# Optimization experiments

Hardware: AMD Instinct MI355X
Metric: run time of the kernel (lower is better)

The kernel has to match this reference:

```python
import jax, jax.numpy as jnp
import numpy as np

BATCH, IN_F, OUT_F = 128, 2048, 512

def setup_inputs() -> dict:
    key = jax.random.key(0)
    k1, k2 = jax.random.split(key)
    m = jax.random.uniform(k1, (BATCH, IN_F), dtype=jnp.float32)
    # weight drawn slightly outside [0,1] so the clamp preprocessing is exercised
    weight = jax.random.uniform(k2, (IN_F, OUT_F), dtype=jnp.float32) * 1.5 - 0.25
    return {"m": m, "weight": weight}

def reference(m, weight):
    # wf = clamp: constrain weights to [0, 1]
    w = jnp.clip(weight, 0.0, 1.0)
    # f = max_min (tropical 'or' composition):
    # out[b, o] = max_i min(m[b, i], w[i, o])
    # broadcast [B, I, 1] with [1, I, O] then reduce over I
    return jnp.max(jnp.minimum(m[:, :, None], w[None, :, :]), axis=1)
```

## Files before the change

### kernel.cpp

```cpp
#include <hip/hip_runtime.h>


__global__ __launch_bounds__(256)
void tmm(const float* __restrict__ M, const float* __restrict__ W,
         float* __restrict__ out) {
    const int t  = threadIdx.x;
    const int wv = __builtin_amdgcn_readfirstlane(t >> 6);
    const int l  = t & 63;
    const int bid = blockIdx.x;
    const int bb = bid & 7;
    const int ob = (bid >> 3) & 7;
    const int ig = bid >> 6;
    const int b0 = bb * 16 + wv * 4;
    const int oc = ob * 64 + l;
    const int i0 = ig * 128;

    const float* Wp = W + i0 * 512 + oc;
    const float* Mp = M + b0 * 2048 + i0;

    float a0 = 0.f, a1 = 0.f, a2 = 0.f, a3 = 0.f;

#pragma unroll 16
    for (int i = 0; i < 128; ++i) {
        float w  = Wp[i * 512];
        float m0 = Mp[i];
        float m1 = Mp[2048 + i];
        float m2 = Mp[4096 + i];
        float m3 = Mp[6144 + i];
        a0 = fmaxf(a0, fminf(m0, w));
        a1 = fmaxf(a1, fminf(m1, w));
        a2 = fmaxf(a2, fminf(m2, w));
        a3 = fmaxf(a3, fminf(m3, w));
    }

    int* o = (int*)out + b0 * 512 + oc;
    atomicMax(o,            __float_as_int(a0));
    atomicMax(o + 512,      __float_as_int(a1));
    atomicMax(o + 1024,     __float_as_int(a2));
    atomicMax(o + 1536,     __float_as_int(a3));
}

extern "C" void kernel_launch(void* const* d_in, const int* in_sizes, int n_in,
                              void* d_out, int out_size, void* d_ws, size_t ws_size,
                              hipStream_t stream) {
    const float* M = (const float*)d_in[0];
    const float* W = (const float*)d_in[1];
    float* out = (float*)d_out;
    tmm<<<dim3(1024), dim3(256), 0, stream>>>(M, W, out);
}
```

Before: 19.49 us.

## Use 2x4 register tile with float4 loads and finer reduction split

Each thread now computes a 2-row by 4-column output tile over a 64-wide slice of the reduction, using float4 loads for both M and W. This raises the number of max/min updates per load and widens memory accesses, aiming to cut load-instruction overhead. The block shape moves to 512 threads across 512 blocks. Halving the reduction slice doubles the number of atomicMax operations on the output, which adds atomic traffic in exchange.

```diff
diff --git a/kernel.cpp b/kernel.cpp
--- a/kernel.cpp
+++ b/kernel.cpp
@@ -1,43 +1,54 @@
 #include <hip/hip_runtime.h>
 
 
-__global__ __launch_bounds__(256)
+#define UPD(acc, mv, wv)                          \
+    acc.x = fmaxf(acc.x, fminf(mv, wv.x));        \
+    acc.y = fmaxf(acc.y, fminf(mv, wv.y));        \
+    acc.z = fmaxf(acc.z, fminf(mv, wv.z));        \
+    acc.w = fmaxf(acc.w, fminf(mv, wv.w));
+
+__global__ __launch_bounds__(512, 4)
 void tmm(const float* __restrict__ M, const float* __restrict__ W,
          float* __restrict__ out) {
     const int t  = threadIdx.x;
-    const int wv = __builtin_amdgcn_readfirstlane(t >> 6);
-    const int l  = t & 63;
+    const int wv = t >> 6, l = t & 63;
     const int bid = blockIdx.x;
     const int bb = bid & 7;
-    const int ob = (bid >> 3) & 7;
-    const int ig = bid >> 6;
-    const int b0 = bb * 16 + wv * 4;
-    const int oc = ob * 64 + l;
-    const int i0 = ig * 128;
+    const int ob = (bid >> 3) & 1;
+    const int ig = bid >> 4;
+    const int r0 = bb * 16 + wv * 2;
+    const int c0 = ob * 256 + l * 4;
+    const int i0 = ig * 64;
 
-    const float* Wp = W + i0 * 512 + oc;
-    const float* Mp = M + b0 * 2048 + i0;
+    const float* Wp = W + (size_t)i0 * 512 + c0;
+    const float* M0 = M + (size_t)r0 * 2048 + i0;
+    const float* M1 = M0 + 2048;
 
-    float a0 = 0.f, a1 = 0.f, a2 = 0.f, a3 = 0.f;
+    float4 a0 = make_float4(0.f, 0.f, 0.f, 0.f);
+    float4 a1 = make_float4(0.f, 0.f, 0.f, 0.f);
 
-#pragma unroll 16
-    for (int i = 0; i < 128; ++i) {
-        float w  = Wp[i * 512];
-        float m0 = Mp[i];
-        float m1 = Mp[2048 + i];
-        float m2 = Mp[4096 + i];
-        float m3 = Mp[6144 + i];
-        a0 = fmaxf(a0, fminf(m0, w));
-        a1 = fmaxf(a1, fminf(m1, w));
-        a2 = fmaxf(a2, fminf(m2, w));
-        a3 = fmaxf(a3, fminf(m3, w));
+#pragma unroll 4
+    for (int i4 = 0; i4 < 16; ++i4) {
+        float4 m0 = *(const float4*)&M0[i4 * 4];
+        float4 m1 = *(const float4*)&M1[i4 * 4];
+        float4 w0 = *(const float4*)&Wp[(i4 * 4 + 0) * 512];
+        float4 w1 = *(const float4*)&Wp[(i4 * 4 + 1) * 512];
+        float4 w2 = *(const float4*)&Wp[(i4 * 4 + 2) * 512];
+        float4 w3 = *(const float4*)&Wp[(i4 * 4 + 3) * 512];
+        UPD(a0, m0.x, w0)  UPD(a0, m0.y, w1)  UPD(a0, m0.z, w2)  UPD(a0, m0.w, w3)
+        UPD(a1, m1.x, w0)  UPD(a1, m1.y, w1)  UPD(a1, m1.z, w2)  UPD(a1, m1.w, w3)
     }
 
-    int* o = (int*)out + b0 * 512 + oc;
-    atomicMax(o,            __float_as_int(a0));
-    atomicMax(o + 512,      __float_as_int(a1));
-    atomicMax(o + 1024,     __float_as_int(a2));
-    atomicMax(o + 1536,     __float_as_int(a3));
+    int* o0 = (int*)out + r0 * 512 + c0;
+    int* o1 = o0 + 512;
+    atomicMax(o0,     __float_as_int(a0.x));
+    atomicMax(o0 + 1, __float_as_int(a0.y));
+    atomicMax(o0 + 2, __float_as_int(a0.z));
+    atomicMax(o0 + 3, __float_as_int(a0.w));
+    atomicMax(o1,     __float_as_int(a1.x));
+    atomicMax(o1 + 1, __float_as_int(a1.y));
+    atomicMax(o1 + 2, __float_as_int(a1.z));
+    atomicMax(o1 + 3, __float_as_int(a1.w));
 }
 
 extern "C" void kernel_launch(void* const* d_in, const int* in_sizes, int n_in,
@@ -46,5 +57,5 @@
     const float* M = (const float*)d_in[0];
     const float* W = (const float*)d_in[1];
     float* out = (float*)d_out;
-    tmm<<<dim3(1024), dim3(256), 0, stream>>>(M, W, out);
+    tmm<<<dim3(512), dim3(512), 0, stream>>>(M, W, out);
 }
```

New measurement: 50.24 us. 2.58x slower.

## Replace split-K atomics with in-block LDS reduction over full K

Applied to the files above, without the earlier changes.

The grid changes from 1024 blocks of 256 threads to 256 blocks of 512 threads. Each block now covers 4 batch rows by 64 outputs over the whole input dimension, with its 8 waves splitting K and combining partial maxima through shared memory. Each output gets one plain store, so the global atomicMax calls and the reliance on a zero-initialised output buffer are gone, and M is read with float4 loads. The cost is less reuse of W: each loaded weight now serves only 4 batch rows instead of 16, which multiplies weight traffic, and there are fewer waves per CU to hide latency.

```diff
diff --git a/kernel.cpp b/kernel.cpp
--- a/kernel.cpp
+++ b/kernel.cpp
@@ -1,43 +1,55 @@
 #include <hip/hip_runtime.h>
 
 
-__global__ __launch_bounds__(256)
+__global__ __launch_bounds__(512)
 void tmm(const float* __restrict__ M, const float* __restrict__ W,
          float* __restrict__ out) {
-    const int t  = threadIdx.x;
-    const int wv = __builtin_amdgcn_readfirstlane(t >> 6);
-    const int l  = t & 63;
+    __shared__ float part[8][4][64];
+    const int t = threadIdx.x;
+    const int c = t & 63;
+    const int s = t >> 6;
     const int bid = blockIdx.x;
-    const int bb = bid & 7;
-    const int ob = (bid >> 3) & 7;
-    const int ig = bid >> 6;
-    const int b0 = bb * 16 + wv * 4;
-    const int oc = ob * 64 + l;
-    const int i0 = ig * 128;
+    const int ot = bid & 7, bt = bid >> 3;
+    const int b0 = bt * 4, o0 = ot * 64;
 
-    const float* Wp = W + i0 * 512 + oc;
-    const float* Mp = M + b0 * 2048 + i0;
+    const float* Wp = W + (size_t)(s * 256) * 512 + o0 + c;
+    const float* Mp = M + (size_t)b0 * 2048 + s * 256;
 
     float a0 = 0.f, a1 = 0.f, a2 = 0.f, a3 = 0.f;
 
-#pragma unroll 16
-    for (int i = 0; i < 128; ++i) {
-        float w  = Wp[i * 512];
-        float m0 = Mp[i];
-        float m1 = Mp[2048 + i];
-        float m2 = Mp[4096 + i];
-        float m3 = Mp[6144 + i];
-        a0 = fmaxf(a0, fminf(m0, w));
-        a1 = fmaxf(a1, fminf(m1, w));
-        a2 = fmaxf(a2, fminf(m2, w));
-        a3 = fmaxf(a3, fminf(m3, w));
+#pragma unroll 2
+    for (int st = 0; st < 64; ++st) {
+        float4 m0 = *(const float4*)&Mp[st * 4];
+        float4 m1 = *(const float4*)&Mp[2048 + st * 4];
+        float4 m2 = *(const float4*)&Mp[4096 + st * 4];
+        float4 m3 = *(const float4*)&Mp[6144 + st * 4];
+        float w0 = Wp[(st * 4 + 0) * 512];
+        float w1 = Wp[(st * 4 + 1) * 512];
+        float w2 = Wp[(st * 4 + 2) * 512];
+        float w3 = Wp[(st * 4 + 3) * 512];
+        a0 = fmaxf(a0, fminf(m0.x, w0)); a1 = fmaxf(a1, fminf(m1.x, w0));
+        a2 = fmaxf(a2, fminf(m2.x, w0)); a3 = fmaxf(a3, fminf(m3.x, w0));
+        a0 = fmaxf(a0, fminf(m0.y, w1)); a1 = fmaxf(a1, fminf(m1.y, w1));
+        a2 = fmaxf(a2, fminf(m2.y, w1)); a3 = fmaxf(a3, fminf(m3.y, w1));
+        a0 = fmaxf(a0, fminf(m0.z, w2)); a1 = fmaxf(a1, fminf(m1.z, w2));
+        a2 = fmaxf(a2, fminf(m2.z, w2)); a3 = fmaxf(a3, fminf(m3.z, w2));
+        a0 = fmaxf(a0, fminf(m0.w, w3)); a1 = fmaxf(a1, fminf(m1.w, w3));
+        a2 = fmaxf(a2, fminf(m2.w, w3)); a3 = fmaxf(a3, fminf(m3.w, w3));
     }
 
-    int* o = (int*)out + b0 * 512 + oc;
-    atomicMax(o,            __float_as_int(a0));
-    atomicMax(o + 512,      __float_as_int(a1));
-    atomicMax(o + 1024,     __float_as_int(a2));
-    atomicMax(o + 1536,     __float_as_int(a3));
+    part[s][0][c] = a0;
+    part[s][1][c] = a1;
+    part[s][2][c] = a2;
+    part[s][3][c] = a3;
+    __syncthreads();
+
+    if (t < 256) {
+        const int r = t >> 6, cc = t & 63;
+        float v = part[0][r][cc];
+#pragma unroll
+        for (int ss = 1; ss < 8; ++ss) v = fmaxf(v, part[ss][r][cc]);
+        out[(b0 + r) * 512 + o0 + cc] = v;
+    }
 }
 
 extern "C" void kernel_launch(void* const* d_in, const int* in_sizes, int n_in,
@@ -46,5 +58,5 @@
     const float* M = (const float*)d_in[0];
     const float* W = (const float*)d_in[1];
     float* out = (float*)d_out;
-    tmm<<<dim3(1024), dim3(256), 0, stream>>>(M, W, out);
+    tmm<<<dim3(256), dim3(512), 0, stream>>>(M, W, out);
 }
```

New measurement: 26.03 us. 1.34x slower.
